# Optimization experiments

Measured on AMD Instinct MI355X. Metric: run time of the kernel, lower is better.

## Reference

```python
import jax, jax.numpy as jnp
import numpy as np

N_NODES = 100000
N_EDGES = 3200000
D_IN = 256
D_OUT = 256


def setup_inputs() -> dict:
    key = jax.random.key(0)
    k1, k2, k3, k4, k5, k6 = jax.random.split(key, 6)
    x = jax.random.normal(k1, (N_NODES, D_IN), dtype=jnp.float32)
    adj_row = jnp.sort(jax.random.randint(k2, (N_EDGES,), 0, N_NODES, dtype=jnp.int64))
    adj_col = jax.random.randint(k3, (N_EDGES,), 0, N_NODES, dtype=jnp.int64)
    adj_val = jax.random.uniform(k4, (N_EDGES,), dtype=jnp.float32)
    stdv = 1.0 / np.sqrt(D_OUT)
    weight = jax.random.uniform(k5, (D_IN, D_OUT), dtype=jnp.float32, minval=-stdv, maxval=stdv)
    bias = jax.random.uniform(k6, (D_OUT,), dtype=jnp.float32, minval=-stdv, maxval=stdv)
    return {"x": x, "adj_row": adj_row, "adj_col": adj_col, "adj_val": adj_val,
            "weight": weight, "bias": bias}


def reference(x, adj_row, adj_col, adj_val, weight, bias):
    # support = x @ W   -> [N, D_OUT]
    support = x @ weight
    # output = spmm(adj, support): gather source rows, scale by edge value,
    # segment-reduce into destination rows.
    msgs = adj_val[:, None] * support[adj_col]          # [E, D_OUT]
    output = jax.ops.segment_sum(msgs, adj_row, num_segments=N_NODES)
    return output + bias
```

## Files before the change

kernel.cpp:

```cpp
#include <hip/hip_runtime.h>
#include <hip/hip_bf16.h>

#define D_FEAT 256

typedef __attribute__((ext_vector_type(8))) __bf16 bf16x8;
typedef __attribute__((ext_vector_type(4))) float f32x4;

__global__ __launch_bounds__(256) void cast_wt(
    const float* __restrict__ W, __bf16* __restrict__ Wt) {
  const int n = blockIdx.x;
  const int k = threadIdx.x;
  Wt[n * 256 + k] = (__bf16)W[k * 256 + n];
}

#define APITCH 40

__global__ __launch_bounds__(256) void gemm_mfma(
    const float* __restrict__ X, const __bf16* __restrict__ Wt,
    __bf16* __restrict__ S, int M) {
  __shared__ __bf16 As[128 * APITCH];
  __shared__ __bf16 Bs[64 * APITCH];
  const int tid = threadIdx.x;
  const int wave = tid >> 6;
  const int lane = tid & 63;
  const int m0 = blockIdx.y * 128;
  const int n0 = blockIdx.x * 64;

  f32x4 acc[2][4] = {};

  const int l15 = lane & 15;
  const int kh8 = (lane >> 4) * 8;

  const int r = tid >> 1;
  const int kh = (tid & 1) * 16;
  const int gr = m0 + r;
  const bool valid = gr < M;
  const float* xsrc = X + (size_t)(valid ? gr : 0) * D_FEAT + kh;

  float4 pre[4];
#pragma unroll
  for (int q = 0; q < 4; ++q)
    pre[q] = valid ? *reinterpret_cast<const float4*>(xsrc + q * 4)
                   : make_float4(0.f, 0.f, 0.f, 0.f);

  const int nr = tid >> 2;
  const int q4 = (tid & 3) * 8;

  for (int k0 = 0; k0 < D_FEAT; k0 += 32) {
    bf16x8 wb = *reinterpret_cast<const bf16x8*>(
        Wt + (size_t)(n0 + nr) * D_FEAT + k0 + q4);

    bf16x8 a0, a1;
    a0[0] = (__bf16)pre[0].x; a0[1] = (__bf16)pre[0].y;
    a0[2] = (__bf16)pre[0].z; a0[3] = (__bf16)pre[0].w;
    a0[4] = (__bf16)pre[1].x; a0[5] = (__bf16)pre[1].y;
    a0[6] = (__bf16)pre[1].z; a0[7] = (__bf16)pre[1].w;
    a1[0] = (__bf16)pre[2].x; a1[1] = (__bf16)pre[2].y;
    a1[2] = (__bf16)pre[2].z; a1[3] = (__bf16)pre[2].w;
    a1[4] = (__bf16)pre[3].x; a1[5] = (__bf16)pre[3].y;
    a1[6] = (__bf16)pre[3].z; a1[7] = (__bf16)pre[3].w;
    *reinterpret_cast<bf16x8*>(&As[r * APITCH + kh]) = a0;
    *reinterpret_cast<bf16x8*>(&As[r * APITCH + kh + 8]) = a1;
    *reinterpret_cast<bf16x8*>(&Bs[nr * APITCH + q4]) = wb;

    const bool have = (k0 + 32) < D_FEAT;
    float4 nxt[4];
    if (have && valid) {
#pragma unroll
      for (int q = 0; q < 4; ++q)
        nxt[q] = *reinterpret_cast<const float4*>(xsrc + k0 + 32 + q * 4);
    }
    __syncthreads();

    bf16x8 a[2], b[4];
#pragma unroll
    for (int rg = 0; rg < 2; ++rg)
      a[rg] = *reinterpret_cast<const bf16x8*>(
          &As[(wave * 32 + rg * 16 + l15) * APITCH + kh8]);
#pragma unroll
    for (int cg = 0; cg < 4; ++cg)
      b[cg] = *reinterpret_cast<const bf16x8*>(
          &Bs[(cg * 16 + l15) * APITCH + kh8]);
#pragma unroll
    for (int rg = 0; rg < 2; ++rg)
#pragma unroll
      for (int cg = 0; cg < 4; ++cg)
        acc[rg][cg] = __builtin_amdgcn_mfma_f32_16x16x32_bf16(
            a[rg], b[cg], acc[rg][cg], 0, 0, 0);
    __syncthreads();

    if (have && valid) {
#pragma unroll
      for (int q = 0; q < 4; ++q) pre[q] = nxt[q];
    }
  }

#pragma unroll
  for (int rg = 0; rg < 2; ++rg) {
    const int rbase = m0 + wave * 32 + rg * 16 + (lane >> 4) * 4;
#pragma unroll
    for (int cg = 0; cg < 4; ++cg) {
      const int c = n0 + cg * 16 + l15;
#pragma unroll
      for (int rr = 0; rr < 4; ++rr) {
        const int row = rbase + rr;
        if (row < M) S[(size_t)row * D_FEAT + c] = (__bf16)acc[rg][cg][rr];
      }
    }
  }
}

__global__ __launch_bounds__(256) void build_rowptr(
    const int* __restrict__ rows, int E, int* __restrict__ ptr, int N) {
  const int n = blockIdx.x * blockDim.x + threadIdx.x;
  if (n > N) return;
  int lo = 0, hi = E;
  while (lo < hi) {
    const int mid = (lo + hi) >> 1;
    if (rows[mid] < n) lo = mid + 1; else hi = mid;
  }
  ptr[n] = lo;
}

__global__ __launch_bounds__(256) void spmm_rows(
    const __bf16* __restrict__ S, const int* __restrict__ ptr,
    const int* __restrict__ col, const float* __restrict__ val,
    const float* __restrict__ bias, float* __restrict__ out, int N) {
  const int wave = threadIdx.x >> 6;
  const int lane = threadIdx.x & 63;
  const int n = blockIdx.x * 4 + wave;
  if (n >= N) return;

  const int e0 = ptr[n];
  const int e1 = ptr[n + 1];
  const int hw = lane >> 5;
  const int l5 = lane & 31;
  const int f0 = l5 * 8;

  float acc[8] = {};
  const int deg = e1 - e0;
  const int nit = (deg + 1) >> 1;

#pragma unroll 4
  for (int it = 0; it < nit; ++it) {
    const int e = e0 + 2 * it + hw;
    int c = 0;
    float v = 0.f;
    if (e < e1) { c = col[e]; v = val[e]; }
    bf16x8 s = *reinterpret_cast<const bf16x8*>(S + (size_t)c * D_FEAT + f0);
#pragma unroll
    for (int j = 0; j < 8; ++j) acc[j] += v * (float)s[j];
  }

#pragma unroll
  for (int j = 0; j < 8; ++j) acc[j] += __shfl(acc[j], lane ^ 32, 64);

  const int fw = f0 + hw * 4;
  const float4 b = *reinterpret_cast<const float4*>(bias + fw);
  const float r0 = hw ? acc[4] : acc[0];
  const float r1 = hw ? acc[5] : acc[1];
  const float r2 = hw ? acc[6] : acc[2];
  const float r3 = hw ? acc[7] : acc[3];
  f32x4 o;
  o[0] = r0 + b.x; o[1] = r1 + b.y; o[2] = r2 + b.z; o[3] = r3 + b.w;
  __builtin_nontemporal_store(
      o, reinterpret_cast<f32x4*>(out + (size_t)n * D_FEAT + fw));
}

extern "C" void kernel_launch(void* const* d_in, const int* in_sizes, int n_in,
                              void* d_out, int out_size, void* d_ws, size_t ws_size,
                              hipStream_t stream) {
  const float* x       = (const float*)d_in[0];
  const int*   adj_row = (const int*)d_in[1];
  const int*   adj_col = (const int*)d_in[2];
  const float* adj_val = (const float*)d_in[3];
  const float* weight  = (const float*)d_in[4];
  const float* bias    = (const float*)d_in[5];
  float*       out     = (float*)d_out;

  const int N = in_sizes[0] / D_FEAT;
  const int E = in_sizes[1];

  __bf16* Wt      = (__bf16*)d_ws;
  __bf16* support = Wt + 256 * 256;
  int*    rowptr  = (int*)(support + (size_t)N * D_FEAT);

  cast_wt<<<256, 256, 0, stream>>>(weight, Wt);

  {
    dim3 grid(D_FEAT / 64, (N + 127) / 128);
    gemm_mfma<<<grid, 256, 0, stream>>>(x, Wt, support, N);
  }
  {
    const int threads = 256;
    const int blocks = (N + 1 + threads - 1) / threads;
    build_rowptr<<<blocks, threads, 0, stream>>>(adj_row, E, rowptr, N);
  }
  {
    const int blocks = (N + 3) / 4;
    spmm_rows<<<blocks, 256, 0, stream>>>(support, rowptr, adj_col, adj_val,
                                          bias, out, N);
  }
}
```

Before: 305.8 us.

## Widen GEMM N-tile to 128 and batch SpMM edge index loads

The GEMM block tile grows from 128x64 to 128x128, so each block loads its slice of X once per two output-column tiles instead of four times. This halves X rereads but doubles the accumulator registers per thread. Separately, the SpMM inner loop now processes edges in batches of 16, loading all column indices and values up front with nontemporal loads. This gives more independent gathers in flight, with a scalar tail loop for leftover edges.

```diff
diff --git a/kernel.cpp b/kernel.cpp
--- a/kernel.cpp
+++ b/kernel.cpp
@@ -19,14 +19,14 @@
     const float* __restrict__ X, const __bf16* __restrict__ Wt,
     __bf16* __restrict__ S, int M) {
   __shared__ __bf16 As[128 * APITCH];
-  __shared__ __bf16 Bs[64 * APITCH];
+  __shared__ __bf16 Bs[128 * APITCH];
   const int tid = threadIdx.x;
   const int wave = tid >> 6;
   const int lane = tid & 63;
   const int m0 = blockIdx.y * 128;
-  const int n0 = blockIdx.x * 64;
-
-  f32x4 acc[2][4] = {};
+  const int n0 = blockIdx.x * 128;
+
+  f32x4 acc[2][8] = {};
 
   const int l15 = lane & 15;
   const int kh8 = (lane >> 4) * 8;
@@ -43,12 +43,13 @@
     pre[q] = valid ? *reinterpret_cast<const float4*>(xsrc + q * 4)
                    : make_float4(0.f, 0.f, 0.f, 0.f);
 
-  const int nr = tid >> 2;
-  const int q4 = (tid & 3) * 8;
+  const int nr = tid >> 1;
+  const int qb = (tid & 1) * 16;
 
   for (int k0 = 0; k0 < D_FEAT; k0 += 32) {
-    bf16x8 wb = *reinterpret_cast<const bf16x8*>(
-        Wt + (size_t)(n0 + nr) * D_FEAT + k0 + q4);
+    const __bf16* wsrc = Wt + (size_t)(n0 + nr) * D_FEAT + k0 + qb;
+    bf16x8 wb0 = *reinterpret_cast<const bf16x8*>(wsrc);
+    bf16x8 wb1 = *reinterpret_cast<const bf16x8*>(wsrc + 8);
 
     bf16x8 a0, a1;
     a0[0] = (__bf16)pre[0].x; a0[1] = (__bf16)pre[0].y;
@@ -61,7 +62,8 @@
     a1[6] = (__bf16)pre[3].z; a1[7] = (__bf16)pre[3].w;
     *reinterpret_cast<bf16x8*>(&As[r * APITCH + kh]) = a0;
     *reinterpret_cast<bf16x8*>(&As[r * APITCH + kh + 8]) = a1;
-    *reinterpret_cast<bf16x8*>(&Bs[nr * APITCH + q4]) = wb;
+    *reinterpret_cast<bf16x8*>(&Bs[nr * APITCH + qb]) = wb0;
+    *reinterpret_cast<bf16x8*>(&Bs[nr * APITCH + qb + 8]) = wb1;
 
     const bool have = (k0 + 32) < D_FEAT;
     float4 nxt[4];
@@ -72,19 +74,19 @@
     }
     __syncthreads();
 
-    bf16x8 a[2], b[4];
+    bf16x8 a[2], b[8];
 #pragma unroll
     for (int rg = 0; rg < 2; ++rg)
       a[rg] = *reinterpret_cast<const bf16x8*>(
           &As[(wave * 32 + rg * 16 + l15) * APITCH + kh8]);
 #pragma unroll
-    for (int cg = 0; cg < 4; ++cg)
+    for (int cg = 0; cg < 8; ++cg)
       b[cg] = *reinterpret_cast<const bf16x8*>(
           &Bs[(cg * 16 + l15) * APITCH + kh8]);
 #pragma unroll
     for (int rg = 0; rg < 2; ++rg)
 #pragma unroll
-      for (int cg = 0; cg < 4; ++cg)
+      for (int cg = 0; cg < 8; ++cg)
         acc[rg][cg] = __builtin_amdgcn_mfma_f32_16x16x32_bf16(
             a[rg], b[cg], acc[rg][cg], 0, 0, 0);
     __syncthreads();
@@ -99,7 +101,7 @@
   for (int rg = 0; rg < 2; ++rg) {
     const int rbase = m0 + wave * 32 + rg * 16 + (lane >> 4) * 4;
 #pragma unroll
-    for (int cg = 0; cg < 4; ++cg) {
+    for (int cg = 0; cg < 8; ++cg) {
       const int c = n0 + cg * 16 + l15;
 #pragma unroll
       for (int rr = 0; rr < 4; ++rr) {
@@ -134,19 +136,34 @@
   const int e0 = ptr[n];
   const int e1 = ptr[n + 1];
   const int hw = lane >> 5;
-  const int l5 = lane & 31;
-  const int f0 = l5 * 8;
+  const int f0 = (lane & 31) * 8;
 
   float acc[8] = {};
   const int deg = e1 - e0;
-  const int nit = (deg + 1) >> 1;
-
-#pragma unroll 4
-  for (int it = 0; it < nit; ++it) {
-    const int e = e0 + 2 * it + hw;
+  const int nb = deg >> 4;
+
+  int e = e0;
+  for (int b = 0; b < nb; ++b) {
+    int cc[8];
+    float vv[8];
+#pragma unroll
+    for (int i = 0; i < 8; ++i) {
+      cc[i] = __builtin_nontemporal_load(col + e + 2 * i + hw);
+      vv[i] = __builtin_nontemporal_load(val + e + 2 * i + hw);
+    }
+#pragma unroll
+    for (int i = 0; i < 8; ++i) {
+      bf16x8 s = *reinterpret_cast<const bf16x8*>(S + (size_t)cc[i] * D_FEAT + f0);
+#pragma unroll
+      for (int j = 0; j < 8; ++j) acc[j] += vv[i] * (float)s[j];
+    }
+    e += 16;
+  }
+  for (; e < e1; e += 2) {
+    const int ee = e + hw;
     int c = 0;
     float v = 0.f;
-    if (e < e1) { c = col[e]; v = val[e]; }
+    if (ee < e1) { c = col[ee]; v = val[ee]; }
     bf16x8 s = *reinterpret_cast<const bf16x8*>(S + (size_t)c * D_FEAT + f0);
 #pragma unroll
     for (int j = 0; j < 8; ++j) acc[j] += v * (float)s[j];
@@ -188,7 +205,7 @@
   cast_wt<<<256, 256, 0, stream>>>(weight, Wt);
 
   {
-    dim3 grid(D_FEAT / 64, (N + 127) / 128);
+    dim3 grid(D_FEAT / 128, (N + 127) / 128);
     gemm_mfma<<<grid, 256, 0, stream>>>(x, Wt, support, N);
   }
   {
```

Measured after the change: 294.7 us. 1.04x faster.
